# Kernel optimization log

Hardware: AMD Instinct MI355X
Metric: run time of the kernel (lower is better)

Reference implementation:

```python
import jax, jax.numpy as jnp
import numpy as np

PAD = -2.0 ** 16 + 1.0  # tf code uses -2**16+1 as masked logit
ITERATIONS = 3


def squash(x):
    # x: [..., out_units]
    n = jnp.sum(jnp.square(x), axis=-1, keepdims=True)
    return (n / (1.0 + n) / jnp.sqrt(n + 1e-9)) * x


def setup_inputs() -> dict:
    key = jax.random.key(0)
    k1, k2, k3, k4 = jax.random.split(key, 4)
    B, L, DIN, DOUT, K = 4096, 200, 64, 64, 8
    return {
        "low_capsule": jax.random.normal(k1, (B, L, DIN), dtype=jnp.float32),
        "seq_len": jax.random.randint(k2, (B, 1), 1, L + 1, dtype=jnp.int32),
        "B_matrix": jax.random.normal(k3, (1, K, L), dtype=jnp.float32),
        "S_matrix": jax.random.normal(k4, (DIN, DOUT), dtype=jnp.float32),
    }


def reference(low_capsule, seq_len, B_matrix, S_matrix):
    # low_capsule: [B, L, Din]; seq_len: [B, 1]; B_matrix: [1, K, L]; S_matrix: [Din, Dout]
    L = B_matrix.shape[2]
    # tf.sequence_mask(tile(seq_len,[1,K]), L) -> [B, K, L]; K axis broadcasts.
    mask = jnp.arange(L)[None, None, :] < seq_len[:, :, None]  # [B, 1, L]
    # low_capsule_new is identical every iteration; compute once.
    low_new = jnp.einsum('bli,io->blo', low_capsule, S_matrix)  # [B, L, Dout]
    Bc = B_matrix  # routing logits, updated (stateful assign_add in tf)
    high = None
    for _ in range(ITERATIONS):
        logits = jnp.where(mask, Bc, PAD)  # [B, K, L]
        W = jax.nn.softmax(logits, axis=-1)
        high = squash(jnp.einsum('bkl,blo->bko', W, low_new))  # [B, K, Dout]
        # B_delta = sum_b high @ low_new^T, keepdims on batch
        Bc = Bc + jnp.einsum('bko,blo->kl', high, low_new)[None]  # [1, K, L]
    return high
```

## Files before the change

### kernel.cpp

```cpp
#include <hip/hip_runtime.h>
#include <math.h>


#define B_SZ  4096
#define L_SZ  200
#define DINK  64
#define DOUTK 64
#define K_SZ  8

__global__ __launch_bounds__(256) void k_init(const float* __restrict__ Bm,
                                              const float* __restrict__ S,
                                              float* __restrict__ Bc,
                                              float* __restrict__ St) {
    int i = blockIdx.x * 256 + threadIdx.x;
    if (i < K_SZ * L_SZ) Bc[i] = Bm[i];
    int j = i - K_SZ * L_SZ;
    if (j >= 0 && j < DINK * DOUTK) {
        int o = j >> 6, ii = j & 63;
        St[j] = S[ii * DOUTK + o];
    }
}

template<int WRITE_OUT>
__global__ __launch_bounds__(256) void k_route(const float* __restrict__ lc_g,
                                               const int* __restrict__ seq_len,
                                               const float* __restrict__ S_g,
                                               const float* __restrict__ St_g,
                                               const float* __restrict__ Bc,
                                               float* __restrict__ partial,
                                               float* __restrict__ out) {
    __shared__ float W_s[K_SZ][L_SZ];
    __shared__ float hp_s[K_SZ][DINK];
    __shared__ float ovl[4 * K_SZ * DINK];
    float (*hp_part)[K_SZ][DINK] = (float (*)[K_SZ][DINK])ovl;
    float (*hx_s)[DINK] = (float (*)[DINK])(ovl);
    float (*hs_s)[DINK] = (float (*)[DINK])(ovl + K_SZ * DINK);

    int t = threadIdx.x;
    int b = blockIdx.x;
    long lbase = (long)b * (L_SZ * DINK);
    const float* lcb = lc_g + lbase;
    const float2* lc2 = (const float2*)lcb;
    int sl = seq_len[b];
    int k = t >> 5, g = t & 31;
    int w = t >> 6;
    int sub = (t >> 5) & 1;
    int p = t & 31;

    const float* bk = Bc + k * L_SZ;
    float m = -3.4e38f;
    for (int l = g; l < sl; l += 32) m = fmaxf(m, bk[l]);
    #pragma unroll
    for (int s = 16; s; s >>= 1) m = fmaxf(m, __shfl_xor(m, s, 32));
    float sum = 0.f;
    for (int l = g; l < sl; l += 32) {
        float e = __expf(bk[l] - m);
        sum += e;
        W_s[k][l] = e;
    }
    #pragma unroll
    for (int s = 16; s; s >>= 1) sum += __shfl_xor(sum, s, 32);
    float rinv = 1.0f / sum;
    __syncthreads();

    {
        float2 acc[K_SZ];
        #pragma unroll
        for (int kk = 0; kk < K_SZ; ++kk) acc[kk] = make_float2(0.f, 0.f);
        int l0 = 2 * w + sub;
        int n = (sl - l0 + 7) >> 3;
        const float2* src = lc2 + l0 * 32 + p;
        for (int j = 0; j < n; ++j) {
            float2 v = src[j * 256];
            int l = l0 + 8 * j;
            #pragma unroll
            for (int kk = 0; kk < K_SZ; ++kk) {
                float wv = W_s[kk][l];
                acc[kk].x += wv * v.x; acc[kk].y += wv * v.y;
            }
        }
        #pragma unroll
        for (int kk = 0; kk < K_SZ; ++kk) {
            acc[kk].x += __shfl_xor(acc[kk].x, 32, 64);
            acc[kk].y += __shfl_xor(acc[kk].y, 32, 64);
        }
        if (sub == 0) {
            #pragma unroll
            for (int kk = 0; kk < K_SZ; ++kk)
                *(float2*)&hp_part[w][kk][2 * p] = acc[kk];
        }
    }
    __syncthreads();

    {
        float2 r = make_float2(0.f, 0.f);
        #pragma unroll
        for (int cc = 0; cc < 4; ++cc) {
            float2 q = *(const float2*)&hp_part[cc][k][2 * g];
            r.x += q.x; r.y += q.y;
        }
        *(float2*)&hp_s[k][2 * g] = make_float2(r.x * rinv, r.y * rinv);
    }
    __syncthreads();

    {
        float h0 = 0.f, h1 = 0.f;
        const float* sp = S_g + 2 * g;
        #pragma unroll 8
        for (int i = 0; i < DINK; ++i) {
            float pv = hp_s[k][i];
            float2 sv = *(const float2*)(sp + i * DOUTK);
            h0 += pv * sv.x; h1 += pv * sv.y;
        }
        float nn = h0 * h0 + h1 * h1;
        #pragma unroll
        for (int s = 16; s; s >>= 1) nn += __shfl_xor(nn, s, 32);
        float sc = nn / ((1.0f + nn) * sqrtf(nn + 1e-9f));
        h0 *= sc; h1 *= sc;
        if (WRITE_OUT) {
            float2* ob2 = (float2*)(out + (long)b * (K_SZ * DOUTK) + k * DOUTK);
            ob2[g] = make_float2(h0, h1);
            return;
        }
        *(float2*)&hx_s[k][2 * g] = make_float2(h0, h1);
    }

    {
        float s0 = 0.f, s1 = 0.f;
        const float* stp = St_g + 2 * g;
        #pragma unroll 8
        for (int o = 0; o < DOUTK; ++o) {
            float hv = hx_s[k][o];
            float2 sv = *(const float2*)(stp + o * DINK);
            s0 += hv * sv.x; s1 += hv * sv.y;
        }
        *(float2*)&hs_s[k][2 * g] = make_float2(s0, s1);
    }
    __syncthreads();

    if (t < L_SZ) {
        const float4* row4 = (const float4*)(lcb + (long)t * DINK);
        float* pb = partial + (long)b * (K_SZ * L_SZ);
        float acc[K_SZ] = {};
        #pragma unroll
        for (int i4 = 0; i4 < 16; ++i4) {
            float4 v = row4[i4];
            #pragma unroll
            for (int kk = 0; kk < K_SZ; ++kk) {
                float4 h = *(const float4*)&hs_s[kk][i4 * 4];
                acc[kk] += v.x * h.x + v.y * h.y + v.z * h.z + v.w * h.w;
            }
        }
        #pragma unroll
        for (int kk = 0; kk < K_SZ; ++kk)
            pb[kk * L_SZ + t] = acc[kk];
    }
}

__global__ __launch_bounds__(256) void k_reduceA(const float* __restrict__ partial,
                                                 float* __restrict__ partial2) {
    __shared__ float red[256];
    int x = blockIdx.x % 50;
    int y = blockIdx.x / 50;
    int t = threadIdx.x;
    int i = x * 32 + (t & 31);
    int sub = t >> 5;
    float s = 0.f;
    for (int p = y * 256 + sub; p < (y + 1) * 256; p += 8)
        s += partial[(long)p * (K_SZ * L_SZ) + i];
    red[t] = s;
    __syncthreads();
    for (int step = 4; step >= 1; step >>= 1) {
        if (sub < step) red[t] += red[t + step * 32];
        __syncthreads();
    }
    if (sub == 0) partial2[y * (K_SZ * L_SZ) + i] = red[t];
}

__global__ __launch_bounds__(256) void k_reduceB(const float* __restrict__ partial2,
                                                 float* __restrict__ Bc) {
    int i = blockIdx.x * 256 + threadIdx.x;
    if (i < K_SZ * L_SZ) {
        float s = 0.f;
        #pragma unroll
        for (int y = 0; y < 16; ++y) s += partial2[y * (K_SZ * L_SZ) + i];
        Bc[i] += s;
    }
}

extern "C" void kernel_launch(void* const* d_in, const int* in_sizes, int n_in,
                              void* d_out, int out_size, void* d_ws, size_t ws_size,
                              hipStream_t stream) {
    const float* lc = (const float*)d_in[0];
    const int*   sl = (const int*)d_in[1];
    const float* Bm = (const float*)d_in[2];
    const float* S  = (const float*)d_in[3];
    float* out = (float*)d_out;
    float* ws  = (float*)d_ws;

    float* Bc      = ws;
    float* St      = ws + 1600;
    float* partial = St + 4096;
    float* p2      = out;

    k_init<<<23, 256, 0, stream>>>(Bm, S, Bc, St);

    k_route<0><<<B_SZ, 256, 0, stream>>>(lc, sl, S, St, Bc, partial, out);
    k_reduceA <<<800, 256, 0, stream>>>(partial, p2);
    k_reduceB <<<7, 256, 0, stream>>>(p2, Bc);
    k_route<0><<<B_SZ, 256, 0, stream>>>(lc, sl, S, St, Bc, partial, out);
    k_reduceA <<<800, 256, 0, stream>>>(partial, p2);
    k_reduceB <<<7, 256, 0, stream>>>(p2, Bc);
    k_route<1><<<B_SZ, 256, 0, stream>>>(lc, sl, S, St, Bc, partial, out);
}
```

Baseline: 289.7 us.

## Split routing kernel into weighted-sum and delta kernels, use fixed-length loops

Splits the fused per-batch routing kernel into k_hp, which computes the weighted sum, squash and S^T projection and writes hs to global memory, and k_delta, which reloads the low capsules to compute the routing-logit partials. The softmax and weighted-sum loops now run a fixed L iterations, with masked weights set to zero, instead of stopping at seq_len, presumably to allow unrolling and more regular memory access. The cost is a second full read of the large input per iteration, an extra hs round trip through global memory, and wasted work on padded positions.

```diff
diff --git a/kernel.cpp b/kernel.cpp
--- a/kernel.cpp
+++ b/kernel.cpp
@@ -22,25 +22,22 @@
 }
 
 template<int WRITE_OUT>
-__global__ __launch_bounds__(256) void k_route(const float* __restrict__ lc_g,
-                                               const int* __restrict__ seq_len,
-                                               const float* __restrict__ S_g,
-                                               const float* __restrict__ St_g,
-                                               const float* __restrict__ Bc,
-                                               float* __restrict__ partial,
-                                               float* __restrict__ out) {
+__global__ __launch_bounds__(256) void k_hp(const float* __restrict__ lc_g,
+                                            const int* __restrict__ seq_len,
+                                            const float* __restrict__ S_g,
+                                            const float* __restrict__ St_g,
+                                            const float* __restrict__ Bc,
+                                            float* __restrict__ hs_g,
+                                            float* __restrict__ out) {
     __shared__ float W_s[K_SZ][L_SZ];
+    __shared__ float ovl[4 * K_SZ * DINK];
     __shared__ float hp_s[K_SZ][DINK];
-    __shared__ float ovl[4 * K_SZ * DINK];
     float (*hp_part)[K_SZ][DINK] = (float (*)[K_SZ][DINK])ovl;
-    float (*hx_s)[DINK] = (float (*)[DINK])(ovl);
-    float (*hs_s)[DINK] = (float (*)[DINK])(ovl + K_SZ * DINK);
+    float (*hx_s)[DINK] = (float (*)[DINK])ovl;
 
     int t = threadIdx.x;
     int b = blockIdx.x;
-    long lbase = (long)b * (L_SZ * DINK);
-    const float* lcb = lc_g + lbase;
-    const float2* lc2 = (const float2*)lcb;
+    const float2* lc2 = (const float2*)(lc_g + (long)b * (L_SZ * DINK));
     int sl = seq_len[b];
     int k = t >> 5, g = t & 31;
     int w = t >> 6;
@@ -53,10 +50,12 @@
     #pragma unroll
     for (int s = 16; s; s >>= 1) m = fmaxf(m, __shfl_xor(m, s, 32));
     float sum = 0.f;
-    for (int l = g; l < sl; l += 32) {
-        float e = __expf(bk[l] - m);
-        sum += e;
-        W_s[k][l] = e;
+    for (int l = g; l < L_SZ + 24; l += 32) {
+        if (l < L_SZ) {
+            float e = (l < sl) ? __expf(bk[l] - m) : 0.f;
+            sum += e;
+            W_s[k][l] = e;
+        }
     }
     #pragma unroll
     for (int s = 16; s; s >>= 1) sum += __shfl_xor(sum, s, 32);
@@ -68,9 +67,9 @@
         #pragma unroll
         for (int kk = 0; kk < K_SZ; ++kk) acc[kk] = make_float2(0.f, 0.f);
         int l0 = 2 * w + sub;
-        int n = (sl - l0 + 7) >> 3;
         const float2* src = lc2 + l0 * 32 + p;
-        for (int j = 0; j < n; ++j) {
+        #pragma unroll 5
+        for (int j = 0; j < 25; ++j) {
             float2 v = src[j * 256];
             int l = l0 + 8 * j;
             #pragma unroll
@@ -103,8 +102,8 @@
     }
     __syncthreads();
 
-    {
-        float h0 = 0.f, h1 = 0.f;
+    float h0 = 0.f, h1 = 0.f;
+    {
         const float* sp = S_g + 2 * g;
         #pragma unroll 8
         for (int i = 0; i < DINK; ++i) {
@@ -117,13 +116,13 @@
         for (int s = 16; s; s >>= 1) nn += __shfl_xor(nn, s, 32);
         float sc = nn / ((1.0f + nn) * sqrtf(nn + 1e-9f));
         h0 *= sc; h1 *= sc;
-        if (WRITE_OUT) {
-            float2* ob2 = (float2*)(out + (long)b * (K_SZ * DOUTK) + k * DOUTK);
-            ob2[g] = make_float2(h0, h1);
-            return;
-        }
-        *(float2*)&hx_s[k][2 * g] = make_float2(h0, h1);
-    }
+    }
+    if (WRITE_OUT) {
+        float2* ob2 = (float2*)(out + (long)b * (K_SZ * DOUTK) + k * DOUTK);
+        ob2[g] = make_float2(h0, h1);
+        return;
+    }
+    *(float2*)&hx_s[k][2 * g] = make_float2(h0, h1);
 
     {
         float s0 = 0.f, s1 = 0.f;
@@ -134,15 +133,26 @@
             float2 sv = *(const float2*)(stp + o * DINK);
             s0 += hv * sv.x; s1 += hv * sv.y;
         }
-        *(float2*)&hs_s[k][2 * g] = make_float2(s0, s1);
-    }
+        float2* hb2 = (float2*)(hs_g + (long)b * (K_SZ * DINK) + k * DINK);
+        hb2[g] = make_float2(s0, s1);
+    }
+}
+
+__global__ __launch_bounds__(256) void k_delta(const float* __restrict__ lc_g,
+                                               const float* __restrict__ hs_g,
+                                               float* __restrict__ partial) {
+    __shared__ float hs_s[K_SZ][DINK];
+    int t = threadIdx.x;
+    int b = blockIdx.x;
+    ((float2*)hs_s)[t] = ((const float2*)(hs_g + (long)b * (K_SZ * DINK)))[t];
     __syncthreads();
 
     if (t < L_SZ) {
-        const float4* row4 = (const float4*)(lcb + (long)t * DINK);
+        const float4* row4 = (const float4*)(lc_g + (long)b * (L_SZ * DINK)
+                                             + (long)t * DINK);
         float* pb = partial + (long)b * (K_SZ * L_SZ);
         float acc[K_SZ] = {};
-        #pragma unroll
+        #pragma unroll 4
         for (int i4 = 0; i4 < 16; ++i4) {
             float4 v = row4[i4];
             #pragma unroll
@@ -199,17 +209,22 @@
     float* ws  = (float*)d_ws;
 
     float* Bc      = ws;
-    float* St      = ws + 1600;
-    float* partial = St + 4096;
+    float* St      = Bc + 1600;
+    float* hs      = St + 4096;
+    float* partial = hs + (long)B_SZ * K_SZ * DINK;
     float* p2      = out;
 
     k_init<<<23, 256, 0, stream>>>(Bm, S, Bc, St);
 
-    k_route<0><<<B_SZ, 256, 0, stream>>>(lc, sl, S, St, Bc, partial, out);
-    k_reduceA <<<800, 256, 0, stream>>>(partial, p2);
-    k_reduceB <<<7, 256, 0, stream>>>(p2, Bc);
-    k_route<0><<<B_SZ, 256, 0, stream>>>(lc, sl, S, St, Bc, partial, out);
-    k_reduceA <<<800, 256, 0, stream>>>(partial, p2);
-    k_reduceB <<<7, 256, 0, stream>>>(p2, Bc);
-    k_route<1><<<B_SZ, 256, 0, stream>>>(lc, sl, S, St, Bc, partial, out);
-}
+    k_hp<0>  <<<B_SZ, 256, 0, stream>>>(lc, sl, S, St, Bc, hs, out);
+    k_delta  <<<B_SZ, 256, 0, stream>>>(lc, hs, partial);
+    k_reduceA<<<800, 256, 0, stream>>>(partial, p2);
+    k_reduceB<<<7, 256, 0, stream>>>(p2, Bc);
+
+    k_hp<0>  <<<B_SZ, 256, 0, stream>>>(lc, sl, S, St, Bc, hs, out);
+    k_delta  <<<B_SZ, 256, 0, stream>>>(lc, hs, partial);
+    k_reduceA<<<800, 256, 0, stream>>>(partial, p2);
+    k_reduceB<<<7, 256, 0, stream>>>(p2, Bc);
+
+    k_hp<1>  <<<B_SZ, 256, 0, stream>>>(lc, sl, S, St, Bc, hs, out);
+}
```

Result: slower. 347.3 us (+19.9%).

## Split softmax into separate kernel and use fixed-length aggregation loop

Applied to the files above, without the earlier changes.

Moves the masked softmax into a separate kernel that writes normalized routing weights to a global buffer, which the routing kernel loads into shared memory. The aggregation loop now always runs over the full sequence length with zero weights for masked positions, giving a fixed trip count that can be unrolled. Normalization is folded into the weights, and one barrier is removed. It adds global traffic for the weight buffer, extra kernel launches, and extra reads of masked input rows.

```diff
diff --git a/kernel.cpp b/kernel.cpp
--- a/kernel.cpp
+++ b/kernel.cpp
@@ -21,31 +21,14 @@
     }
 }
 
-template<int WRITE_OUT>
-__global__ __launch_bounds__(256) void k_route(const float* __restrict__ lc_g,
-                                               const int* __restrict__ seq_len,
-                                               const float* __restrict__ S_g,
-                                               const float* __restrict__ St_g,
-                                               const float* __restrict__ Bc,
-                                               float* __restrict__ partial,
-                                               float* __restrict__ out) {
+__global__ __launch_bounds__(256) void k_soft(const int* __restrict__ seq_len,
+                                              const float* __restrict__ Bc,
+                                              float* __restrict__ W_g) {
     __shared__ float W_s[K_SZ][L_SZ];
-    __shared__ float hp_s[K_SZ][DINK];
-    __shared__ float ovl[4 * K_SZ * DINK];
-    float (*hp_part)[K_SZ][DINK] = (float (*)[K_SZ][DINK])ovl;
-    float (*hx_s)[DINK] = (float (*)[DINK])(ovl);
-    float (*hs_s)[DINK] = (float (*)[DINK])(ovl + K_SZ * DINK);
-
     int t = threadIdx.x;
     int b = blockIdx.x;
-    long lbase = (long)b * (L_SZ * DINK);
-    const float* lcb = lc_g + lbase;
-    const float2* lc2 = (const float2*)lcb;
+    int k = t >> 5, g = t & 31;
     int sl = seq_len[b];
-    int k = t >> 5, g = t & 31;
-    int w = t >> 6;
-    int sub = (t >> 5) & 1;
-    int p = t & 31;
 
     const float* bk = Bc + k * L_SZ;
     float m = -3.4e38f;
@@ -53,14 +36,50 @@
     #pragma unroll
     for (int s = 16; s; s >>= 1) m = fmaxf(m, __shfl_xor(m, s, 32));
     float sum = 0.f;
-    for (int l = g; l < sl; l += 32) {
-        float e = __expf(bk[l] - m);
+    for (int l = g; l < L_SZ; l += 32) {
+        float e = (l < sl) ? __expf(bk[l] - m) : 0.f;
         sum += e;
         W_s[k][l] = e;
     }
     #pragma unroll
     for (int s = 16; s; s >>= 1) sum += __shfl_xor(sum, s, 32);
     float rinv = 1.0f / sum;
+    for (int l = g; l < L_SZ; l += 32) W_s[k][l] *= rinv;
+    __syncthreads();
+
+    float4* dst = (float4*)(W_g + (long)b * (K_SZ * L_SZ));
+    const float4* src = (const float4*)&W_s[0][0];
+    for (int j = t; j < (K_SZ * L_SZ) / 4; j += 256) dst[j] = src[j];
+}
+
+template<int WRITE_OUT>
+__global__ __launch_bounds__(256) void k_route2(const float* __restrict__ lc_g,
+                                                const float* __restrict__ W_g,
+                                                const float* __restrict__ S_g,
+                                                const float* __restrict__ St_g,
+                                                float* __restrict__ partial,
+                                                float* __restrict__ out) {
+    __shared__ float W_s[K_SZ][L_SZ];
+    __shared__ float ovl[4 * K_SZ * DINK];
+    __shared__ float hp_s[K_SZ][DINK];
+    float (*hp_part)[K_SZ][DINK] = (float (*)[K_SZ][DINK])ovl;
+    float (*hx_s)[DINK] = (float (*)[DINK])ovl;
+    float (*hs_s)[DINK] = (float (*)[DINK])(ovl + K_SZ * DINK);
+
+    int t = threadIdx.x;
+    int b = blockIdx.x;
+    const float* lcb = lc_g + (long)b * (L_SZ * DINK);
+    const float2* lc2 = (const float2*)lcb;
+    int k = t >> 5, g = t & 31;
+    int w = t >> 6;
+    int sub = (t >> 5) & 1;
+    int p = t & 31;
+
+    {
+        const float4* src = (const float4*)(W_g + (long)b * (K_SZ * L_SZ));
+        float4* dst = (float4*)&W_s[0][0];
+        for (int j = t; j < (K_SZ * L_SZ) / 4; j += 256) dst[j] = src[j];
+    }
     __syncthreads();
 
     {
@@ -68,9 +87,9 @@
         #pragma unroll
         for (int kk = 0; kk < K_SZ; ++kk) acc[kk] = make_float2(0.f, 0.f);
         int l0 = 2 * w + sub;
-        int n = (sl - l0 + 7) >> 3;
         const float2* src = lc2 + l0 * 32 + p;
-        for (int j = 0; j < n; ++j) {
+        #pragma unroll 5
+        for (int j = 0; j < 25; ++j) {
             float2 v = src[j * 256];
             int l = l0 + 8 * j;
             #pragma unroll
@@ -99,12 +118,11 @@
             float2 q = *(const float2*)&hp_part[cc][k][2 * g];
             r.x += q.x; r.y += q.y;
         }
-        *(float2*)&hp_s[k][2 * g] = make_float2(r.x * rinv, r.y * rinv);
-    }
-    __syncthreads();
-
-    {
-        float h0 = 0.f, h1 = 0.f;
+        *(float2*)&hp_s[k][2 * g] = r;
+    }
+
+    float h0 = 0.f, h1 = 0.f;
+    {
         const float* sp = S_g + 2 * g;
         #pragma unroll 8
         for (int i = 0; i < DINK; ++i) {
@@ -117,13 +135,13 @@
         for (int s = 16; s; s >>= 1) nn += __shfl_xor(nn, s, 32);
         float sc = nn / ((1.0f + nn) * sqrtf(nn + 1e-9f));
         h0 *= sc; h1 *= sc;
-        if (WRITE_OUT) {
-            float2* ob2 = (float2*)(out + (long)b * (K_SZ * DOUTK) + k * DOUTK);
-            ob2[g] = make_float2(h0, h1);
-            return;
-        }
-        *(float2*)&hx_s[k][2 * g] = make_float2(h0, h1);
-    }
+    }
+    if (WRITE_OUT) {
+        float2* ob2 = (float2*)(out + (long)b * (K_SZ * DOUTK) + k * DOUTK);
+        ob2[g] = make_float2(h0, h1);
+        return;
+    }
+    *(float2*)&hx_s[k][2 * g] = make_float2(h0, h1);
 
     {
         float s0 = 0.f, s1 = 0.f;
@@ -142,7 +160,7 @@
         const float4* row4 = (const float4*)(lcb + (long)t * DINK);
         float* pb = partial + (long)b * (K_SZ * L_SZ);
         float acc[K_SZ] = {};
-        #pragma unroll
+        #pragma unroll 4
         for (int i4 = 0; i4 < 16; ++i4) {
             float4 v = row4[i4];
             #pragma unroll
@@ -199,17 +217,23 @@
     float* ws  = (float*)d_ws;
 
     float* Bc      = ws;
-    float* St      = ws + 1600;
-    float* partial = St + 4096;
+    float* St      = Bc + 1600;
+    float* W       = St + 4096;
+    float* partial = W + (long)B_SZ * K_SZ * L_SZ;
     float* p2      = out;
 
     k_init<<<23, 256, 0, stream>>>(Bm, S, Bc, St);
 
-    k_route<0><<<B_SZ, 256, 0, stream>>>(lc, sl, S, St, Bc, partial, out);
+    k_soft    <<<B_SZ, 256, 0, stream>>>(sl, Bc, W);
+    k_route2<0><<<B_SZ, 256, 0, stream>>>(lc, W, S, St, partial, out);
     k_reduceA <<<800, 256, 0, stream>>>(partial, p2);
     k_reduceB <<<7, 256, 0, stream>>>(p2, Bc);
-    k_route<0><<<B_SZ, 256, 0, stream>>>(lc, sl, S, St, Bc, partial, out);
+
+    k_soft    <<<B_SZ, 256, 0, stream>>>(sl, Bc, W);
+    k_route2<0><<<B_SZ, 256, 0, stream>>>(lc, W, S, St, partial, out);
     k_reduceA <<<800, 256, 0, stream>>>(partial, p2);
     k_reduceB <<<7, 256, 0, stream>>>(p2, Bc);
-    k_route<1><<<B_SZ, 256, 0, stream>>>(lc, sl, S, St, Bc, partial, out);
-}
+
+    k_soft    <<<B_SZ, 256, 0, stream>>>(sl, Bc, W);
+    k_route2<1><<<B_SZ, 256, 0, stream>>>(lc, W, S, St, partial, out);
+}
```

Result: slower. 340.9 us (+17.7%).
